# Kernel optimization log

Hardware: AMD Instinct MI355X
Metric: run time of the kernel (lower is better)

## Reference

```python
import jax, jax.numpy as jnp
import numpy as np
from jax.experimental.ode import odeint

B, T, NV = 2048, 256, 32   # batch, time steps, n ICU variables
H, L, OH = 64, 32, 64      # gru hidden, latent dim, ode hidden


def setup_inputs() -> dict:
    key = jax.random.key(0)
    ks = jax.random.split(key, 24)
    def rn(k, shape, s):
        return (jax.random.normal(k, shape) * s).astype(jnp.float32)
    times = jnp.broadcast_to(jnp.linspace(0.0, 48.0, T, dtype=jnp.float32), (B, T))
    values = jax.random.normal(ks[0], (B, T, NV), dtype=jnp.float32)
    mask = (jax.random.uniform(ks[1], (B, T, NV)) < 0.5).astype(jnp.float32)
    seq_lengths = jnp.sort(jax.random.randint(ks[2], (B,), 1, T + 1))[::-1]
    seq_lengths = seq_lengths.at[0].set(T).astype(jnp.int32)
    eps = jax.random.normal(ks[3], (B, L), dtype=jnp.float32)
    return {
        "times": times, "values": values, "mask": mask,
        "seq_lengths": seq_lengths, "eps": eps,
        # GRU (torch layout: gates stacked r,z,n)
        "W_ih": rn(ks[4], (3 * H, 2 * NV), 0.1), "W_hh": rn(ks[5], (3 * H, H), 0.1),
        "b_ih": rn(ks[6], (3 * H,), 0.05), "b_hh": rn(ks[7], (3 * H,), 0.05),
        # hidden -> z0 params
        "W_z0": rn(ks[8], (2 * L, H), 0.1), "b_z0": rn(ks[9], (2 * L,), 0.05),
        # ODE func MLP (small weights keep dynamics tame for dopri5)
        "ode_W1": rn(ks[10], (OH, L), 0.05), "ode_b1": rn(ks[11], (OH,), 0.02),
        "ode_W2": rn(ks[12], (OH, OH), 0.05), "ode_b2": rn(ks[13], (OH,), 0.02),
        "ode_W3": rn(ks[14], (L, OH), 0.05), "ode_b3": rn(ks[15], (L,), 0.02),
        # decoder
        "dec_W1": rn(ks[16], (H, L), 0.1), "dec_b1": rn(ks[17], (H,), 0.05),
        "dec_W2": rn(ks[18], (1, H), 0.1), "dec_b2": rn(ks[19], (1,), 0.05),
    }


def _latent_ode_fwd(times, values, mask, seq_lengths, eps,
                    W_ih, W_hh, b_ih, b_hh, W_z0, b_z0,
                    ode_W1, ode_b1, ode_W2, ode_b2, ode_W3, ode_b3,
                    dec_W1, dec_b1, dec_W2, dec_b2):
    Bx, Tx = values.shape[0], values.shape[1]
    # encoder: concat (values, mask), flip time, run GRU over first seq_len steps
    x = jnp.concatenate([values, mask], axis=-1)[:, ::-1, :]          # [B,T,2NV]
    xp = jnp.einsum('btf,gf->tbg', x, W_ih) + b_ih                    # [T,B,3H]

    def gru_step(h, inp):
        xpt, t = inp                                                  # xpt: [B,3H]
        hh = h @ W_hh.T + b_hh
        xr, xz, xn = jnp.split(xpt, 3, axis=-1)
        hr, hz, hn = jnp.split(hh, 3, axis=-1)
        r = jax.nn.sigmoid(xr + hr)
        zg = jax.nn.sigmoid(xz + hz)
        n = jnp.tanh(xn + r * hn)
        h_new = (1.0 - zg) * n + zg * h
        h = jnp.where((t < seq_lengths)[:, None], h_new, h)           # packed-seq freeze
        return h, None

    h0 = jnp.zeros((Bx, W_hh.shape[1]), values.dtype)
    h, _ = jax.lax.scan(gru_step, h0, (xp, jnp.arange(Tx)))

    z0p = h @ W_z0.T + b_z0                                           # [B,2L]
    Ld = z0p.shape[-1] // 2
    z0_mean, z0_logvar = z0p[:, :Ld], z0p[:, Ld:]
    z0 = z0_mean + eps * jnp.exp(0.5 * z0_logvar)                     # reparameterize

    def ode_f(z, t, p):
        W1, b1, W2, b2, W3, b3 = p
        hl = jnp.tanh(z @ W1.T + b1)
        hl = jnp.tanh(hl @ W2.T + b2)
        return hl @ W3.T + b3

    t_span = jnp.array([0.0, 48.0], dtype=jnp.float32)
    traj = odeint(ode_f, z0, t_span,
                  (ode_W1, ode_b1, ode_W2, ode_b2, ode_W3, ode_b3),
                  rtol=1e-7, atol=1e-9)                               # dopri5, torchdiffeq defaults
    z_final = traj[-1]

    logits = (jax.nn.relu(z_final @ dec_W1.T + dec_b1) @ dec_W2.T + dec_b2)[:, 0]
    kl = -0.5 * jnp.mean(1.0 + z0_logvar - z0_mean ** 2 - jnp.exp(z0_logvar))
    return logits, kl


def reference(times, values, mask, seq_lengths, eps,
              W_ih, W_hh, b_ih, b_hh, W_z0, b_z0,
              ode_W1, ode_b1, ode_W2, ode_b2, ode_W3, ode_b3,
              dec_W1, dec_b1, dec_W2, dec_b2):
    return _latent_ode_fwd(times, values, mask, seq_lengths, eps,
                           W_ih, W_hh, b_ih, b_hh, W_z0, b_z0,
                           ode_W1, ode_b1, ode_W2, ode_b2, ode_W3, ode_b3,
                           dec_W1, dec_b1, dec_W2, dec_b2)
```

## Files before the change

kernel.cpp:

```cpp
#include <hip/hip_runtime.h>

#define B_ 2048
#define T_ 256
#define NV_ 32
#define H_ 64
#define L_ 32
#define OH_ 64
#define NSTEP 16

typedef _Float16 f16x8 __attribute__((ext_vector_type(8)));
typedef _Float16 f16x4 __attribute__((ext_vector_type(4)));
typedef _Float16 f16x2 __attribute__((ext_vector_type(2)));
typedef float f32x4 __attribute__((ext_vector_type(4)));

#define MFMA16(a, b, c) __builtin_amdgcn_mfma_f32_16x16x32_f16((a), (b), (c), 0, 0, 0)

__device__ __forceinline__ float rcp_(float x) { return __builtin_amdgcn_rcpf(x); }
__device__ __forceinline__ float sigm(float x) { return rcp_(1.0f + __expf(-x)); }
__device__ __forceinline__ float tanh_(float x) { return 2.0f * rcp_(1.0f + __expf(-2.0f * x)) - 1.0f; }

__device__ __forceinline__ f16x8 pack8(f32x4 a, f32x4 b) {
    f16x8 r;
    r[0] = (_Float16)a[0]; r[1] = (_Float16)a[1]; r[2] = (_Float16)a[2]; r[3] = (_Float16)a[3];
    r[4] = (_Float16)b[0]; r[5] = (_Float16)b[1]; r[6] = (_Float16)b[2]; r[7] = (_Float16)b[3];
    return r;
}

__global__ __launch_bounds__(256) void gru_kernel(
    const float* __restrict__ values, const float* __restrict__ mask,
    const int* __restrict__ seql, const float* __restrict__ eps,
    const float* __restrict__ W_ih, const float* __restrict__ W_hh,
    const float* __restrict__ b_ih, const float* __restrict__ b_hh,
    const float* __restrict__ W_z0, const float* __restrict__ b_z0,
    float* __restrict__ z0ws, float* __restrict__ parts)
{
    const int tid = threadIdx.x;
    const int w   = tid >> 6;
    const int l   = tid & 63;
    const int c   = l & 15;
    const int g4  = l >> 4;
    const int b0  = blockIdx.x * 16;

    __shared__ unsigned h_u32[2][16][36];
    __shared__ float    zp_lds[16][65];
    __shared__ float    red_lds[4];

    for (int i = tid; i < 2 * 16 * 36; i += 256) (&h_u32[0][0][0])[i] = 0u;

    f16x8 bih[3][2], bhh[3][2];
#pragma unroll
    for (int gate = 0; gate < 3; ++gate) {
#pragma unroll
        for (int kt = 0; kt < 2; ++kt) {
            const float* p1 = W_ih + (gate * 64 + w * 16 + c) * 64 + kt * 32 + g4 * 8;
            bih[gate][kt] = pack8(*(const f32x4*)p1, *(const f32x4*)(p1 + 4));
            const float* p2 = W_hh + (gate * 64 + w * 16 + c) * 64 + kt * 32 + g4 * 8;
            bhh[gate][kt] = pack8(*(const f32x4*)p2, *(const f32x4*)(p2 + 4));
        }
    }

    f32x4 bRq, bZq, bNXq, bNHq;
#pragma unroll
    for (int r = 0; r < 4; ++r) {
        const int f = w * 16 + g4 * 4 + r;
        bRq[r]  = b_ih[f]       + b_hh[f];
        bZq[r]  = b_ih[64 + f]  + b_hh[64 + f];
        bNXq[r] = b_ih[128 + f];
        bNHq[r] = b_hh[128 + f];
    }

    const int sl_c  = seql[b0 + c];
    const int tmax  = seql[b0];
    float hp[4] = {0.f, 0.f, 0.f, 0.f};

    const float* vrow = values + (size_t)(b0 + c) * T_ * NV_ + g4 * 8;
    const float* mrow = mask   + (size_t)(b0 + c) * T_ * NV_ + g4 * 8;

    f32x4 av0, av1, am0, am1, bv0, bv1, bm0, bm1;
    {
        const float* vp = vrow + (T_ - 1) * NV_;
        const float* mp = mrow + (T_ - 1) * NV_;
        av0 = *(const f32x4*)vp; av1 = *(const f32x4*)(vp + 4);
        am0 = *(const f32x4*)mp; am1 = *(const f32x4*)(mp + 4);
    }
    {
        const int tt = (1 < tmax) ? 1 : 0;
        const float* vp = vrow + (T_ - 1 - tt) * NV_;
        const float* mp = mrow + (T_ - 1 - tt) * NV_;
        bv0 = *(const f32x4*)vp; bv1 = *(const f32x4*)(vp + 4);
        bm0 = *(const f32x4*)mp; bm1 = *(const f32x4*)(mp + 4);
    }

    __syncthreads();

    int cur = 0;

    auto STEP = [&](f32x4& v0, f32x4& v1, f32x4& m0, f32x4& m1, int tc) {
        f16x8 ha0 = *(const f16x8*)&h_u32[cur][c][4 * g4];
        f16x8 ha1 = *(const f16x8*)&h_u32[cur][c][16 + 4 * g4];

        f16x8 xa0 = pack8(v0, v1);
        f16x8 xa1 = pack8(m0, m1);

        const int tt = (tc + 2 < tmax) ? (tc + 2) : 0;
        const float* vp = vrow + (T_ - 1 - tt) * NV_;
        const float* mp = mrow + (T_ - 1 - tt) * NV_;
        v0 = *(const f32x4*)vp; v1 = *(const f32x4*)(vp + 4);
        m0 = *(const f32x4*)mp; m1 = *(const f32x4*)(mp + 4);

        f32x4 accR  = MFMA16(bih[0][0], xa0, bRq);
        f32x4 accNX = MFMA16(bih[2][0], xa0, bNXq);
        f32x4 accZ  = MFMA16(bih[1][0], xa0, bZq);
        accR  = MFMA16(bih[0][1], xa1, accR);
        accNX = MFMA16(bih[2][1], xa1, accNX);
        accZ  = MFMA16(bih[1][1], xa1, accZ);

        f32x4 accNH = MFMA16(bhh[2][0], ha0, bNHq);
        accR  = MFMA16(bhh[0][0], ha0, accR);
        accNH = MFMA16(bhh[2][1], ha1, accNH);
        accR  = MFMA16(bhh[0][1], ha1, accR);
        accZ  = MFMA16(bhh[1][0], ha0, accZ);
        accZ  = MFMA16(bhh[1][1], ha1, accZ);

        const bool act = (tc < sl_c);
#pragma unroll
        for (int r = 0; r < 4; ++r) {
            float rr   = sigm(accR[r]);
            float zz   = sigm(accZ[r]);
            float nn   = tanh_(accNX[r] + rr * accNH[r]);
            float hnew = nn + zz * (hp[r] - nn);
            if (act) hp[r] = hnew;
        }

        const int nxt = cur ^ 1;
        f16x2 q0 = { (_Float16)hp[0], (_Float16)hp[1] };
        f16x2 q1 = { (_Float16)hp[2], (_Float16)hp[3] };
        h_u32[nxt][c][8 * w + 2 * g4]     = __builtin_bit_cast(unsigned, q0);
        h_u32[nxt][c][8 * w + 2 * g4 + 1] = __builtin_bit_cast(unsigned, q1);

        asm volatile("s_waitcnt lgkmcnt(0)\n\ts_barrier" ::: "memory");
        cur = nxt;
    };

    int t = 0;
    while (true) {
        STEP(av0, av1, am0, am1, t);
        if (t + 1 >= tmax) break;
        STEP(bv0, bv1, bm0, bm1, t + 1);
        t += 2;
        if (t >= tmax) break;
    }

    f16x8 az0f[2];
#pragma unroll
    for (int kt = 0; kt < 2; ++kt) {
        const float* p = W_z0 + (w * 16 + c) * 64 + kt * 32 + g4 * 8;
        az0f[kt] = pack8(*(const f32x4*)p, *(const f32x4*)(p + 4));
    }
    f16x8 hf0 = *(const f16x8*)&h_u32[cur][c][4 * g4];
    f16x8 hf1 = *(const f16x8*)&h_u32[cur][c][16 + 4 * g4];
    f32x4 az;
#pragma unroll
    for (int r = 0; r < 4; ++r) az[r] = b_z0[w * 16 + g4 * 4 + r];
    az = MFMA16(az0f[0], hf0, az);
    az = MFMA16(az0f[1], hf1, az);
#pragma unroll
    for (int r = 0; r < 4; ++r) zp_lds[c][w * 16 + g4 * 4 + r] = az[r];
    __syncthreads();

    const int row = tid >> 4;
    const int j2  = (tid & 15) * 2;
    float m0 = zp_lds[row][j2],      m1 = zp_lds[row][j2 + 1];
    float v0 = zp_lds[row][32 + j2], v1 = zp_lds[row][32 + j2 + 1];
    const float* erow = eps + (size_t)(b0 + row) * L_;
    float e0 = erow[j2], e1 = erow[j2 + 1];
    float* zrow = z0ws + (size_t)(b0 + row) * L_;
    float s0 = __expf(0.5f * v0), s1 = __expf(0.5f * v1);
    zrow[j2]     = m0 + e0 * s0;
    zrow[j2 + 1] = m1 + e1 * s1;
    float kls = (1.0f + v0 - m0 * m0 - s0 * s0) + (1.0f + v1 - m1 * m1 - s1 * s1);
#pragma unroll
    for (int off = 32; off >= 1; off >>= 1) kls += __shfl_down(kls, off);
    if (l == 0) red_lds[w] = kls;
    __syncthreads();
    if (tid == 0) parts[blockIdx.x] = red_lds[0] + red_lds[1] + red_lds[2] + red_lds[3];
}

__global__ __launch_bounds__(64) void ode_kernel(
    const float* __restrict__ z0ws,
    const float* __restrict__ oW1, const float* __restrict__ ob1,
    const float* __restrict__ oW2, const float* __restrict__ ob2,
    const float* __restrict__ oW3, const float* __restrict__ ob3,
    const float* __restrict__ dW1, const float* __restrict__ db1,
    const float* __restrict__ dW2, const float* __restrict__ db2,
    float* __restrict__ out)
{
    const int l  = threadIdx.x;
    const int c  = l & 15;
    const int g4 = l >> 4;
    const int b0 = blockIdx.x * 16;

    __shared__ _Float16 zbuf[16][40];
    __shared__ _Float16 buf1[16][72];
    __shared__ _Float16 buf2[16][72];

    f16x8 w1f[4], d1f[4], w2f[4][2], w3f[2][2];
#pragma unroll
    for (int mt = 0; mt < 4; ++mt) {
        const float* p = oW1 + (mt * 16 + c) * 32 + g4 * 8;
        w1f[mt] = pack8(*(const f32x4*)p, *(const f32x4*)(p + 4));
        const float* q = dW1 + (mt * 16 + c) * 32 + g4 * 8;
        d1f[mt] = pack8(*(const f32x4*)q, *(const f32x4*)(q + 4));
#pragma unroll
        for (int kt = 0; kt < 2; ++kt) {
            const float* r = oW2 + (mt * 16 + c) * 64 + kt * 32 + g4 * 8;
            w2f[mt][kt] = pack8(*(const f32x4*)r, *(const f32x4*)(r + 4));
        }
    }
#pragma unroll
    for (int mt = 0; mt < 2; ++mt) {
#pragma unroll
        for (int kt = 0; kt < 2; ++kt) {
            const float* r = oW3 + (mt * 16 + c) * 64 + kt * 32 + g4 * 8;
            w3f[mt][kt] = pack8(*(const f32x4*)r, *(const f32x4*)(r + 4));
        }
    }

    f32x4 b1q[4], b2q[4], d1q[4], w2q[4], b3q[2];
#pragma unroll
    for (int mt = 0; mt < 4; ++mt) {
#pragma unroll
        for (int r = 0; r < 4; ++r) {
            b1q[mt][r] = ob1[mt * 16 + g4 * 4 + r];
            b2q[mt][r] = ob2[mt * 16 + g4 * 4 + r];
            d1q[mt][r] = db1[mt * 16 + g4 * 4 + r];
            w2q[mt][r] = dW2[mt * 16 + g4 * 4 + r];
        }
    }
#pragma unroll
    for (int mt = 0; mt < 2; ++mt) {
#pragma unroll
        for (int r = 0; r < 4; ++r) b3q[mt][r] = ob3[mt * 16 + g4 * 4 + r];
    }
    const float bd2 = db2[0];

    f32x4 z[2];
#pragma unroll
    for (int mt = 0; mt < 2; ++mt)
        z[mt] = *(const f32x4*)(z0ws + (size_t)(b0 + c) * L_ + mt * 16 + g4 * 4);

    auto evalf = [&](const f32x4* zin, f32x4* kout) {
#pragma unroll
        for (int mt = 0; mt < 2; ++mt) {
            f16x4 hv;
#pragma unroll
            for (int r = 0; r < 4; ++r) hv[r] = (_Float16)zin[mt][r];
            *(f16x4*)&zbuf[c][mt * 16 + g4 * 4] = hv;
        }
        f16x8 zf = *(const f16x8*)&zbuf[c][g4 * 8];

        f32x4 h1[4];
#pragma unroll
        for (int mt = 0; mt < 4; ++mt) h1[mt] = MFMA16(w1f[mt], zf, b1q[mt]);
#pragma unroll
        for (int mt = 0; mt < 4; ++mt) {
            f16x4 hv;
#pragma unroll
            for (int r = 0; r < 4; ++r) hv[r] = (_Float16)tanh_(h1[mt][r]);
            *(f16x4*)&buf1[c][mt * 16 + g4 * 4] = hv;
        }
        f16x8 a1 = *(const f16x8*)&buf1[c][g4 * 8];
        f16x8 a2 = *(const f16x8*)&buf1[c][32 + g4 * 8];

        f32x4 h2[4];
#pragma unroll
        for (int mt = 0; mt < 4; ++mt) {
            h2[mt] = MFMA16(w2f[mt][0], a1, b2q[mt]);
            h2[mt] = MFMA16(w2f[mt][1], a2, h2[mt]);
        }
#pragma unroll
        for (int mt = 0; mt < 4; ++mt) {
            f16x4 hv;
#pragma unroll
            for (int r = 0; r < 4; ++r) hv[r] = (_Float16)tanh_(h2[mt][r]);
            *(f16x4*)&buf2[c][mt * 16 + g4 * 4] = hv;
        }
        f16x8 a3 = *(const f16x8*)&buf2[c][g4 * 8];
        f16x8 a4 = *(const f16x8*)&buf2[c][32 + g4 * 8];

#pragma unroll
        for (int mt = 0; mt < 2; ++mt) {
            kout[mt] = MFMA16(w3f[mt][0], a3, b3q[mt]);
            kout[mt] = MFMA16(w3f[mt][1], a4, kout[mt]);
        }
    };

    const float dt = 48.0f / (float)NSTEP;
    for (int s = 0; s < NSTEP; ++s) {
        f32x4 k[2], ks[2], zt[2];
        evalf(z, k);
#pragma unroll
        for (int mt = 0; mt < 2; ++mt) { ks[mt] = k[mt]; zt[mt] = z[mt] + k[mt] * (0.5f * dt); }
        evalf(zt, k);
#pragma unroll
        for (int mt = 0; mt < 2; ++mt) { ks[mt] += k[mt] * 2.0f; zt[mt] = z[mt] + k[mt] * (0.5f * dt); }
        evalf(zt, k);
#pragma unroll
        for (int mt = 0; mt < 2; ++mt) { ks[mt] += k[mt] * 2.0f; zt[mt] = z[mt] + k[mt] * dt; }
        evalf(zt, k);
#pragma unroll
        for (int mt = 0; mt < 2; ++mt) z[mt] += (ks[mt] + k[mt]) * (dt / 6.0f);
    }

#pragma unroll
    for (int mt = 0; mt < 2; ++mt) {
        f16x4 hv;
#pragma unroll
        for (int r = 0; r < 4; ++r) hv[r] = (_Float16)z[mt][r];
        *(f16x4*)&zbuf[c][mt * 16 + g4 * 4] = hv;
    }
    f16x8 zf = *(const f16x8*)&zbuf[c][g4 * 8];
    float p = 0.0f;
#pragma unroll
    for (int mt = 0; mt < 4; ++mt) {
        f32x4 d = MFMA16(d1f[mt], zf, d1q[mt]);
#pragma unroll
        for (int r = 0; r < 4; ++r) p += fmaxf(d[r], 0.0f) * w2q[mt][r];
    }
    p += __shfl_xor(p, 16);
    p += __shfl_xor(p, 32);
    if (l < 16) out[b0 + c] = p + bd2;
}

__global__ __launch_bounds__(128) void kl_fin(const float* __restrict__ parts,
                                              float* __restrict__ out)
{
    __shared__ float sred[2];
    const int tid = threadIdx.x;
    float p = parts[tid];
#pragma unroll
    for (int off = 32; off >= 1; off >>= 1) p += __shfl_down(p, off);
    if ((tid & 63) == 0) sred[tid >> 6] = p;
    __syncthreads();
    if (tid == 0) out[B_] = -0.5f * (sred[0] + sred[1]) / (float)(B_ * L_);
}

extern "C" void kernel_launch(void* const* d_in, const int* in_sizes, int n_in,
                              void* d_out, int out_size, void* d_ws, size_t ws_size,
                              hipStream_t stream) {
    const float* values = (const float*)d_in[1];
    const float* mask   = (const float*)d_in[2];
    const int*   seql   = (const int*)d_in[3];
    const float* eps    = (const float*)d_in[4];
    const float* W_ih   = (const float*)d_in[5];
    const float* W_hh   = (const float*)d_in[6];
    const float* b_ih   = (const float*)d_in[7];
    const float* b_hh   = (const float*)d_in[8];
    const float* W_z0   = (const float*)d_in[9];
    const float* b_z0   = (const float*)d_in[10];
    const float* oW1    = (const float*)d_in[11];
    const float* ob1    = (const float*)d_in[12];
    const float* oW2    = (const float*)d_in[13];
    const float* ob2    = (const float*)d_in[14];
    const float* oW3    = (const float*)d_in[15];
    const float* ob3    = (const float*)d_in[16];
    const float* dW1    = (const float*)d_in[17];
    const float* db1    = (const float*)d_in[18];
    const float* dW2    = (const float*)d_in[19];
    const float* db2    = (const float*)d_in[20];
    float* out = (float*)d_out;

    float* z0ws  = (float*)d_ws;
    float* parts = z0ws + (size_t)B_ * L_;

    hipLaunchKernelGGL(gru_kernel, dim3(B_ / 16), dim3(256), 0, stream,
                       values, mask, seql, eps, W_ih, W_hh, b_ih, b_hh, W_z0, b_z0,
                       z0ws, parts);
    hipLaunchKernelGGL(ode_kernel, dim3(B_ / 16), dim3(64), 0, stream,
                       z0ws, oW1, ob1, oW2, ob2, oW3, ob3, dW1, db1, dW2, db2, out);
    hipLaunchKernelGGL(kl_fin, dim3(1), dim3(128), 0, stream, parts, out);
}
```

Before: 202.0 us.

## Split GRU into producer/consumer waves overlapping input projection with recurrence

Doubles the GRU block to 512 threads. Four producer waves load the inputs and compute the input-projection MFMAs one step ahead into a double-buffered LDS array. Four consumer waves run only the hidden-state MFMAs and gate math, raising their priority with s_setprio, which takes the input projection off the serial recurrence's critical path. The cost is extra LDS traffic, a barrier shared by twice as many waves, and half the threads idle during the epilogue.

```diff
diff --git a/kernel.cpp b/kernel.cpp
--- a/kernel.cpp
+++ b/kernel.cpp
@@ -26,7 +26,9 @@
     return r;
 }
 
-__global__ __launch_bounds__(256) void gru_kernel(
+#define RAWBAR() asm volatile("s_waitcnt lgkmcnt(0)\n\ts_barrier" ::: "memory")
+
+__global__ __launch_bounds__(512) void gru_kernel(
     const float* __restrict__ values, const float* __restrict__ mask,
     const int* __restrict__ seql, const float* __restrict__ eps,
     const float* __restrict__ W_ih, const float* __restrict__ W_hh,
@@ -34,154 +36,188 @@
     const float* __restrict__ W_z0, const float* __restrict__ b_z0,
     float* __restrict__ z0ws, float* __restrict__ parts)
 {
-    const int tid = threadIdx.x;
-    const int w   = tid >> 6;
-    const int l   = tid & 63;
-    const int c   = l & 15;
-    const int g4  = l >> 4;
-    const int b0  = blockIdx.x * 16;
+    const int tid  = threadIdx.x;
+    const int wave = tid >> 6;
+    const int l    = tid & 63;
+    const int c    = l & 15;
+    const int g4   = l >> 4;
+    const int b0   = blockIdx.x * 16;
+    const int w    = wave & 3;
+    const bool producer = (wave < 4);
 
     __shared__ unsigned h_u32[2][16][36];
-    __shared__ float    zp_lds[16][65];
+    __shared__ float    xp[2][16][200];
+    __shared__ float    zp_lds[16][68];
     __shared__ float    red_lds[4];
 
-    for (int i = tid; i < 2 * 16 * 36; i += 256) (&h_u32[0][0][0])[i] = 0u;
-
-    f16x8 bih[3][2], bhh[3][2];
-#pragma unroll
-    for (int gate = 0; gate < 3; ++gate) {
-#pragma unroll
-        for (int kt = 0; kt < 2; ++kt) {
-            const float* p1 = W_ih + (gate * 64 + w * 16 + c) * 64 + kt * 32 + g4 * 8;
-            bih[gate][kt] = pack8(*(const f32x4*)p1, *(const f32x4*)(p1 + 4));
-            const float* p2 = W_hh + (gate * 64 + w * 16 + c) * 64 + kt * 32 + g4 * 8;
-            bhh[gate][kt] = pack8(*(const f32x4*)p2, *(const f32x4*)(p2 + 4));
-        }
-    }
-
-    f32x4 bRq, bZq, bNXq, bNHq;
-#pragma unroll
-    for (int r = 0; r < 4; ++r) {
-        const int f = w * 16 + g4 * 4 + r;
-        bRq[r]  = b_ih[f]       + b_hh[f];
-        bZq[r]  = b_ih[64 + f]  + b_hh[64 + f];
-        bNXq[r] = b_ih[128 + f];
-        bNHq[r] = b_hh[128 + f];
-    }
-
-    const int sl_c  = seql[b0 + c];
-    const int tmax  = seql[b0];
-    float hp[4] = {0.f, 0.f, 0.f, 0.f};
-
+    for (int i = tid; i < 2 * 16 * 36; i += 512) (&h_u32[0][0][0])[i] = 0u;
+
+    const int tmax = seql[b0];
+
+    f16x8 bih[3][2];
+    f32x4 bRq, bZq, bNXq;
+    f32x4 av0, av1, am0, am1, bv0, bv1, bm0, bm1;
     const float* vrow = values + (size_t)(b0 + c) * T_ * NV_ + g4 * 8;
     const float* mrow = mask   + (size_t)(b0 + c) * T_ * NV_ + g4 * 8;
 
-    f32x4 av0, av1, am0, am1, bv0, bv1, bm0, bm1;
-    {
-        const float* vp = vrow + (T_ - 1) * NV_;
-        const float* mp = mrow + (T_ - 1) * NV_;
-        av0 = *(const f32x4*)vp; av1 = *(const f32x4*)(vp + 4);
-        am0 = *(const f32x4*)mp; am1 = *(const f32x4*)(mp + 4);
-    }
-    {
-        const int tt = (1 < tmax) ? 1 : 0;
-        const float* vp = vrow + (T_ - 1 - tt) * NV_;
-        const float* mp = mrow + (T_ - 1 - tt) * NV_;
-        bv0 = *(const f32x4*)vp; bv1 = *(const f32x4*)(vp + 4);
-        bm0 = *(const f32x4*)mp; bm1 = *(const f32x4*)(mp + 4);
+    f16x8 bhh[3][2];
+    f32x4 bNHq;
+    int   sl_c = 0;
+    float hp[4] = {0.f, 0.f, 0.f, 0.f};
+
+    if (producer) {
+#pragma unroll
+        for (int gate = 0; gate < 3; ++gate) {
+#pragma unroll
+            for (int kt = 0; kt < 2; ++kt) {
+                const float* p1 = W_ih + (gate * 64 + w * 16 + c) * 64 + kt * 32 + g4 * 8;
+                bih[gate][kt] = pack8(*(const f32x4*)p1, *(const f32x4*)(p1 + 4));
+            }
+        }
+#pragma unroll
+        for (int r = 0; r < 4; ++r) {
+            const int f = w * 16 + g4 * 4 + r;
+            bRq[r]  = b_ih[f]       + b_hh[f];
+            bZq[r]  = b_ih[64 + f]  + b_hh[64 + f];
+            bNXq[r] = b_ih[128 + f];
+        }
+        {
+            const float* vp = vrow + (T_ - 1) * NV_;
+            const float* mp = mrow + (T_ - 1) * NV_;
+            av0 = *(const f32x4*)vp; av1 = *(const f32x4*)(vp + 4);
+            am0 = *(const f32x4*)mp; am1 = *(const f32x4*)(mp + 4);
+        }
+        {
+            const int tt = (1 < tmax) ? 1 : 0;
+            const float* vp = vrow + (T_ - 1 - tt) * NV_;
+            const float* mp = mrow + (T_ - 1 - tt) * NV_;
+            bv0 = *(const f32x4*)vp; bv1 = *(const f32x4*)(vp + 4);
+            bm0 = *(const f32x4*)mp; bm1 = *(const f32x4*)(mp + 4);
+        }
+    } else {
+#pragma unroll
+        for (int gate = 0; gate < 3; ++gate) {
+#pragma unroll
+            for (int kt = 0; kt < 2; ++kt) {
+                const float* p2 = W_hh + (gate * 64 + w * 16 + c) * 64 + kt * 32 + g4 * 8;
+                bhh[gate][kt] = pack8(*(const f32x4*)p2, *(const f32x4*)(p2 + 4));
+            }
+        }
+#pragma unroll
+        for (int r = 0; r < 4; ++r) bNHq[r] = b_hh[128 + w * 16 + g4 * 4 + r];
+        sl_c = seql[b0 + c];
     }
 
     __syncthreads();
 
-    int cur = 0;
-
-    auto STEP = [&](f32x4& v0, f32x4& v1, f32x4& m0, f32x4& m1, int tc) {
-        f16x8 ha0 = *(const f16x8*)&h_u32[cur][c][4 * g4];
-        f16x8 ha1 = *(const f16x8*)&h_u32[cur][c][16 + 4 * g4];
-
+    const int xoff = w * 16 + g4 * 4;
+
+    auto PROD = [&](f32x4& v0, f32x4& v1, f32x4& m0, f32x4& m1, int p) {
         f16x8 xa0 = pack8(v0, v1);
         f16x8 xa1 = pack8(m0, m1);
-
-        const int tt = (tc + 2 < tmax) ? (tc + 2) : 0;
+        const int tt = (p + 2 < tmax) ? (p + 2) : 0;
         const float* vp = vrow + (T_ - 1 - tt) * NV_;
         const float* mp = mrow + (T_ - 1 - tt) * NV_;
         v0 = *(const f32x4*)vp; v1 = *(const f32x4*)(vp + 4);
         m0 = *(const f32x4*)mp; m1 = *(const f32x4*)(mp + 4);
 
-        f32x4 accR  = MFMA16(bih[0][0], xa0, bRq);
-        f32x4 accNX = MFMA16(bih[2][0], xa0, bNXq);
-        f32x4 accZ  = MFMA16(bih[1][0], xa0, bZq);
-        accR  = MFMA16(bih[0][1], xa1, accR);
-        accNX = MFMA16(bih[2][1], xa1, accNX);
-        accZ  = MFMA16(bih[1][1], xa1, accZ);
-
+        f32x4 aR  = MFMA16(bih[0][0], xa0, bRq);
+        f32x4 aZ  = MFMA16(bih[1][0], xa0, bZq);
+        f32x4 aNX = MFMA16(bih[2][0], xa0, bNXq);
+        aR  = MFMA16(bih[0][1], xa1, aR);
+        aZ  = MFMA16(bih[1][1], xa1, aZ);
+        aNX = MFMA16(bih[2][1], xa1, aNX);
+
+        float* dst = &xp[p & 1][c][0];
+        *(f32x4*)(dst + xoff)       = aR;
+        *(f32x4*)(dst + 64 + xoff)  = aZ;
+        *(f32x4*)(dst + 128 + xoff) = aNX;
+    };
+
+    auto CONS = [&](int t, int cur) {
+        const float* src = &xp[t & 1][c][0];
+        f32x4 xpR  = *(const f32x4*)(src + xoff);
+        f32x4 xpZ  = *(const f32x4*)(src + 64 + xoff);
+        f32x4 xpNX = *(const f32x4*)(src + 128 + xoff);
+        f16x8 ha0 = *(const f16x8*)&h_u32[cur][c][4 * g4];
+        f16x8 ha1 = *(const f16x8*)&h_u32[cur][c][16 + 4 * g4];
+
+        __builtin_amdgcn_s_setprio(1);
+        f32x4 accR  = MFMA16(bhh[0][0], ha0, xpR);
         f32x4 accNH = MFMA16(bhh[2][0], ha0, bNHq);
-        accR  = MFMA16(bhh[0][0], ha0, accR);
+        f32x4 accZ  = MFMA16(bhh[1][0], ha0, xpZ);
+        accR  = MFMA16(bhh[0][1], ha1, accR);
         accNH = MFMA16(bhh[2][1], ha1, accNH);
-        accR  = MFMA16(bhh[0][1], ha1, accR);
-        accZ  = MFMA16(bhh[1][0], ha0, accZ);
         accZ  = MFMA16(bhh[1][1], ha1, accZ);
 
-        const bool act = (tc < sl_c);
+        const bool act = (t < sl_c);
 #pragma unroll
         for (int r = 0; r < 4; ++r) {
             float rr   = sigm(accR[r]);
             float zz   = sigm(accZ[r]);
-            float nn   = tanh_(accNX[r] + rr * accNH[r]);
+            float nn   = tanh_(xpNX[r] + rr * accNH[r]);
             float hnew = nn + zz * (hp[r] - nn);
             if (act) hp[r] = hnew;
         }
-
-        const int nxt = cur ^ 1;
-        f16x2 q0 = { (_Float16)hp[0], (_Float16)hp[1] };
-        f16x2 q1 = { (_Float16)hp[2], (_Float16)hp[3] };
-        h_u32[nxt][c][8 * w + 2 * g4]     = __builtin_bit_cast(unsigned, q0);
-        h_u32[nxt][c][8 * w + 2 * g4 + 1] = __builtin_bit_cast(unsigned, q1);
-
-        asm volatile("s_waitcnt lgkmcnt(0)\n\ts_barrier" ::: "memory");
-        cur = nxt;
+        __builtin_amdgcn_s_setprio(0);
+
+        f16x4 hq;
+#pragma unroll
+        for (int r = 0; r < 4; ++r) hq[r] = (_Float16)hp[r];
+        *(f16x4*)&h_u32[cur ^ 1][c][8 * w + 2 * g4] = hq;
     };
 
-    int t = 0;
+    if (producer) PROD(av0, av1, am0, am1, 0);
+    RAWBAR();
+
+    int t = 0, cur = 0;
     while (true) {
-        STEP(av0, av1, am0, am1, t);
-        if (t + 1 >= tmax) break;
-        STEP(bv0, bv1, bm0, bm1, t + 1);
-        t += 2;
+        if (producer) { if (t + 1 < tmax) PROD(bv0, bv1, bm0, bm1, t + 1); }
+        else          CONS(t, cur);
+        RAWBAR();
+        cur ^= 1; ++t;
         if (t >= tmax) break;
-    }
-
-    f16x8 az0f[2];
-#pragma unroll
-    for (int kt = 0; kt < 2; ++kt) {
-        const float* p = W_z0 + (w * 16 + c) * 64 + kt * 32 + g4 * 8;
-        az0f[kt] = pack8(*(const f32x4*)p, *(const f32x4*)(p + 4));
-    }
-    f16x8 hf0 = *(const f16x8*)&h_u32[cur][c][4 * g4];
-    f16x8 hf1 = *(const f16x8*)&h_u32[cur][c][16 + 4 * g4];
-    f32x4 az;
-#pragma unroll
-    for (int r = 0; r < 4; ++r) az[r] = b_z0[w * 16 + g4 * 4 + r];
-    az = MFMA16(az0f[0], hf0, az);
-    az = MFMA16(az0f[1], hf1, az);
-#pragma unroll
-    for (int r = 0; r < 4; ++r) zp_lds[c][w * 16 + g4 * 4 + r] = az[r];
+        if (producer) { if (t + 1 < tmax) PROD(av0, av1, am0, am1, t + 1); }
+        else          CONS(t, cur);
+        RAWBAR();
+        cur ^= 1; ++t;
+        if (t >= tmax) break;
+    }
+
+    if (!producer) {
+        f16x8 az0f[2];
+#pragma unroll
+        for (int kt = 0; kt < 2; ++kt) {
+            const float* p = W_z0 + (w * 16 + c) * 64 + kt * 32 + g4 * 8;
+            az0f[kt] = pack8(*(const f32x4*)p, *(const f32x4*)(p + 4));
+        }
+        f16x8 hf0 = *(const f16x8*)&h_u32[cur][c][4 * g4];
+        f16x8 hf1 = *(const f16x8*)&h_u32[cur][c][16 + 4 * g4];
+        f32x4 az;
+#pragma unroll
+        for (int r = 0; r < 4; ++r) az[r] = b_z0[w * 16 + g4 * 4 + r];
+        az = MFMA16(az0f[0], hf0, az);
+        az = MFMA16(az0f[1], hf1, az);
+        *(f32x4*)&zp_lds[c][xoff] = az;
+    }
     __syncthreads();
 
-    const int row = tid >> 4;
-    const int j2  = (tid & 15) * 2;
-    float m0 = zp_lds[row][j2],      m1 = zp_lds[row][j2 + 1];
-    float v0 = zp_lds[row][32 + j2], v1 = zp_lds[row][32 + j2 + 1];
-    const float* erow = eps + (size_t)(b0 + row) * L_;
-    float e0 = erow[j2], e1 = erow[j2 + 1];
-    float* zrow = z0ws + (size_t)(b0 + row) * L_;
-    float s0 = __expf(0.5f * v0), s1 = __expf(0.5f * v1);
-    zrow[j2]     = m0 + e0 * s0;
-    zrow[j2 + 1] = m1 + e1 * s1;
-    float kls = (1.0f + v0 - m0 * m0 - s0 * s0) + (1.0f + v1 - m1 * m1 - s1 * s1);
-#pragma unroll
-    for (int off = 32; off >= 1; off >>= 1) kls += __shfl_down(kls, off);
-    if (l == 0) red_lds[w] = kls;
+    if (tid < 256) {
+        const int row = tid >> 4;
+        const int j2  = (tid & 15) * 2;
+        float m0 = zp_lds[row][j2],      m1 = zp_lds[row][j2 + 1];
+        float v0 = zp_lds[row][32 + j2], v1 = zp_lds[row][32 + j2 + 1];
+        const float* erow = eps + (size_t)(b0 + row) * L_;
+        float e0 = erow[j2], e1 = erow[j2 + 1];
+        float* zrow = z0ws + (size_t)(b0 + row) * L_;
+        float s0 = __expf(0.5f * v0), s1 = __expf(0.5f * v1);
+        zrow[j2]     = m0 + e0 * s0;
+        zrow[j2 + 1] = m1 + e1 * s1;
+        float kls = (1.0f + v0 - m0 * m0 - s0 * s0) + (1.0f + v1 - m1 * m1 - s1 * s1);
+#pragma unroll
+        for (int off = 32; off >= 1; off >>= 1) kls += __shfl_down(kls, off);
+        if (l == 0) red_lds[wave] = kls;
+    }
     __syncthreads();
     if (tid == 0) parts[blockIdx.x] = red_lds[0] + red_lds[1] + red_lds[2] + red_lds[3];
 }
@@ -373,7 +409,7 @@
     float* z0ws  = (float*)d_ws;
     float* parts = z0ws + (size_t)B_ * L_;
 
-    hipLaunchKernelGGL(gru_kernel, dim3(B_ / 16), dim3(256), 0, stream,
+    hipLaunchKernelGGL(gru_kernel, dim3(B_ / 16), dim3(512), 0, stream,
                        values, mask, seql, eps, W_ih, W_hh, b_ih, b_hh, W_z0, b_z0,
                        z0ws, parts);
     hipLaunchKernelGGL(ode_kernel, dim3(B_ / 16), dim3(64), 0, stream,
```

New measurement: 194.3 us. 3.8% less time.

## Replace GRU step barrier with LDS counter spin-wait and deepen input prefetch

Applied to the files above, without the earlier changes.

Swaps the per-timestep s_barrier in the GRU recurrence for an LDS atomic counter that each wave bumps and then spin-waits on. Input prefetch is deepened from 2 to 6 timesteps using six register sets, so global load latency is hidden further ahead. Hidden-state writes are merged into a single f16x4 store and the z-projection into a single vector store. The spin loop adds LDS polling traffic, the extra prefetch sets raise register pressure, and correctness now rests on the counter ordering standing in for the barrier.

```diff
diff --git a/kernel.cpp b/kernel.cpp
--- a/kernel.cpp
+++ b/kernel.cpp
@@ -7,10 +7,10 @@
 #define L_ 32
 #define OH_ 64
 #define NSTEP 16
+#define DEPTH 6
 
 typedef _Float16 f16x8 __attribute__((ext_vector_type(8)));
 typedef _Float16 f16x4 __attribute__((ext_vector_type(4)));
-typedef _Float16 f16x2 __attribute__((ext_vector_type(2)));
 typedef float f32x4 __attribute__((ext_vector_type(4)));
 
 #define MFMA16(a, b, c) __builtin_amdgcn_mfma_f32_16x16x32_f16((a), (b), (c), 0, 0, 0)
@@ -42,10 +42,12 @@
     const int b0  = blockIdx.x * 16;
 
     __shared__ unsigned h_u32[2][16][36];
-    __shared__ float    zp_lds[16][65];
+    __shared__ float    zp_lds[16][68];
     __shared__ float    red_lds[4];
+    __shared__ unsigned cnt;
 
     for (int i = tid; i < 2 * 16 * 36; i += 256) (&h_u32[0][0][0])[i] = 0u;
+    if (tid == 0) cnt = 0u;
 
     f16x8 bih[3][2], bhh[3][2];
 #pragma unroll
@@ -69,86 +71,77 @@
         bNHq[r] = b_hh[128 + f];
     }
 
-    const int sl_c  = seql[b0 + c];
-    const int tmax  = seql[b0];
+    const int sl_c = seql[b0 + c];
+    const int tmax = seql[b0];
     float hp[4] = {0.f, 0.f, 0.f, 0.f};
 
     const float* vrow = values + (size_t)(b0 + c) * T_ * NV_ + g4 * 8;
     const float* mrow = mask   + (size_t)(b0 + c) * T_ * NV_ + g4 * 8;
 
-    f32x4 av0, av1, am0, am1, bv0, bv1, bm0, bm1;
-    {
-        const float* vp = vrow + (T_ - 1) * NV_;
-        const float* mp = mrow + (T_ - 1) * NV_;
-        av0 = *(const f32x4*)vp; av1 = *(const f32x4*)(vp + 4);
-        am0 = *(const f32x4*)mp; am1 = *(const f32x4*)(mp + 4);
-    }
-    {
-        const int tt = (1 < tmax) ? 1 : 0;
-        const float* vp = vrow + (T_ - 1 - tt) * NV_;
-        const float* mp = mrow + (T_ - 1 - tt) * NV_;
-        bv0 = *(const f32x4*)vp; bv1 = *(const f32x4*)(vp + 4);
-        bm0 = *(const f32x4*)mp; bm1 = *(const f32x4*)(mp + 4);
-    }
+#define DECLSET(S) f32x4 S##v0, S##v1, S##m0, S##m1
+    DECLSET(A); DECLSET(B); DECLSET(C); DECLSET(D); DECLSET(E); DECLSET(F);
+#define FILLSET(S, tc) do {                                                  \
+        const int tt_ = ((tc) < tmax) ? (tc) : 0;                            \
+        const float* vp_ = vrow + (T_ - 1 - tt_) * NV_;                      \
+        const float* mp_ = mrow + (T_ - 1 - tt_) * NV_;                      \
+        S##v0 = *(const f32x4*)vp_; S##v1 = *(const f32x4*)(vp_ + 4);        \
+        S##m0 = *(const f32x4*)mp_; S##m1 = *(const f32x4*)(mp_ + 4);        \
+    } while (0)
+    FILLSET(A, 0); FILLSET(B, 1); FILLSET(C, 2);
+    FILLSET(D, 3); FILLSET(E, 4); FILLSET(F, 5);
 
     __syncthreads();
 
-    int cur = 0;
-
-    auto STEP = [&](f32x4& v0, f32x4& v1, f32x4& m0, f32x4& m1, int tc) {
-        f16x8 ha0 = *(const f16x8*)&h_u32[cur][c][4 * g4];
-        f16x8 ha1 = *(const f16x8*)&h_u32[cur][c][16 + 4 * g4];
-
-        f16x8 xa0 = pack8(v0, v1);
-        f16x8 xa1 = pack8(m0, m1);
-
-        const int tt = (tc + 2 < tmax) ? (tc + 2) : 0;
-        const float* vp = vrow + (T_ - 1 - tt) * NV_;
-        const float* mp = mrow + (T_ - 1 - tt) * NV_;
-        v0 = *(const f32x4*)vp; v1 = *(const f32x4*)(vp + 4);
-        m0 = *(const f32x4*)mp; m1 = *(const f32x4*)(mp + 4);
-
-        f32x4 accR  = MFMA16(bih[0][0], xa0, bRq);
-        f32x4 accNX = MFMA16(bih[2][0], xa0, bNXq);
-        f32x4 accZ  = MFMA16(bih[1][0], xa0, bZq);
-        accR  = MFMA16(bih[0][1], xa1, accR);
-        accNX = MFMA16(bih[2][1], xa1, accNX);
-        accZ  = MFMA16(bih[1][1], xa1, accZ);
-
-        f32x4 accNH = MFMA16(bhh[2][0], ha0, bNHq);
-        accR  = MFMA16(bhh[0][0], ha0, accR);
-        accNH = MFMA16(bhh[2][1], ha1, accNH);
-        accR  = MFMA16(bhh[0][1], ha1, accR);
-        accZ  = MFMA16(bhh[1][0], ha0, accZ);
-        accZ  = MFMA16(bhh[1][1], ha1, accZ);
-
-        const bool act = (tc < sl_c);
-#pragma unroll
-        for (int r = 0; r < 4; ++r) {
-            float rr   = sigm(accR[r]);
-            float zz   = sigm(accZ[r]);
-            float nn   = tanh_(accNX[r] + rr * accNH[r]);
-            float hnew = nn + zz * (hp[r] - nn);
-            if (act) hp[r] = hnew;
-        }
-
-        const int nxt = cur ^ 1;
-        f16x2 q0 = { (_Float16)hp[0], (_Float16)hp[1] };
-        f16x2 q1 = { (_Float16)hp[2], (_Float16)hp[3] };
-        h_u32[nxt][c][8 * w + 2 * g4]     = __builtin_bit_cast(unsigned, q0);
-        h_u32[nxt][c][8 * w + 2 * g4 + 1] = __builtin_bit_cast(unsigned, q1);
-
-        asm volatile("s_waitcnt lgkmcnt(0)\n\ts_barrier" ::: "memory");
-        cur = nxt;
-    };
+#define GSTEP(S, tc) do {                                                    \
+        f16x8 ha0 = *(const f16x8*)&h_u32[(tc) & 1][c][4 * g4];              \
+        f16x8 ha1 = *(const f16x8*)&h_u32[(tc) & 1][c][16 + 4 * g4];         \
+        f16x8 xa0 = pack8(S##v0, S##v1);                                     \
+        f16x8 xa1 = pack8(S##m0, S##m1);                                     \
+        FILLSET(S, (tc) + DEPTH);                                            \
+        f32x4 accR  = MFMA16(bih[0][0], xa0, bRq);                           \
+        f32x4 accNX = MFMA16(bih[2][0], xa0, bNXq);                          \
+        f32x4 accZ  = MFMA16(bih[1][0], xa0, bZq);                           \
+        accR  = MFMA16(bih[0][1], xa1, accR);                                \
+        accNX = MFMA16(bih[2][1], xa1, accNX);                               \
+        accZ  = MFMA16(bih[1][1], xa1, accZ);                                \
+        f32x4 accNH = MFMA16(bhh[2][0], ha0, bNHq);                          \
+        accR  = MFMA16(bhh[0][0], ha0, accR);                                \
+        accNH = MFMA16(bhh[2][1], ha1, accNH);                               \
+        accR  = MFMA16(bhh[0][1], ha1, accR);                                \
+        accZ  = MFMA16(bhh[1][0], ha0, accZ);                                \
+        accZ  = MFMA16(bhh[1][1], ha1, accZ);                                \
+        const bool act = ((tc) < sl_c);                                      \
+        _Pragma("unroll")                                                    \
+        for (int r = 0; r < 4; ++r) {                                        \
+            float rr   = sigm(accR[r]);                                      \
+            float zz   = sigm(accZ[r]);                                      \
+            float nn   = tanh_(accNX[r] + rr * accNH[r]);                    \
+            float hnew = nn + zz * (hp[r] - nn);                             \
+            if (act) hp[r] = hnew;                                           \
+        }                                                                    \
+        f16x4 hq;                                                            \
+        _Pragma("unroll")                                                    \
+        for (int r = 0; r < 4; ++r) hq[r] = (_Float16)hp[r];                 \
+        *(f16x4*)&h_u32[((tc) & 1) ^ 1][c][8 * w + 2 * g4] = hq;             \
+        asm volatile("s_waitcnt lgkmcnt(0)" ::: "memory");                   \
+        if (l == 0) atomicAdd(&cnt, 1u);                                     \
+        asm volatile("" ::: "memory");                                       \
+        {                                                                    \
+            const unsigned tgt_ = 4u * ((unsigned)(tc) + 1u);                \
+            while (__builtin_amdgcn_readfirstlane(                           \
+                       *(volatile unsigned*)&cnt) < tgt_) { }                \
+        }                                                                    \
+        asm volatile("" ::: "memory");                                       \
+    } while (0)
 
     int t = 0;
     while (true) {
-        STEP(av0, av1, am0, am1, t);
-        if (t + 1 >= tmax) break;
-        STEP(bv0, bv1, bm0, bm1, t + 1);
-        t += 2;
-        if (t >= tmax) break;
+        GSTEP(A, t); if (++t >= tmax) break;
+        GSTEP(B, t); if (++t >= tmax) break;
+        GSTEP(C, t); if (++t >= tmax) break;
+        GSTEP(D, t); if (++t >= tmax) break;
+        GSTEP(E, t); if (++t >= tmax) break;
+        GSTEP(F, t); if (++t >= tmax) break;
     }
 
     f16x8 az0f[2];
@@ -157,15 +150,15 @@
         const float* p = W_z0 + (w * 16 + c) * 64 + kt * 32 + g4 * 8;
         az0f[kt] = pack8(*(const f32x4*)p, *(const f32x4*)(p + 4));
     }
-    f16x8 hf0 = *(const f16x8*)&h_u32[cur][c][4 * g4];
-    f16x8 hf1 = *(const f16x8*)&h_u32[cur][c][16 + 4 * g4];
+    const int fin = tmax & 1;
+    f16x8 hf0 = *(const f16x8*)&h_u32[fin][c][4 * g4];
+    f16x8 hf1 = *(const f16x8*)&h_u32[fin][c][16 + 4 * g4];
     f32x4 az;
 #pragma unroll
     for (int r = 0; r < 4; ++r) az[r] = b_z0[w * 16 + g4 * 4 + r];
     az = MFMA16(az0f[0], hf0, az);
     az = MFMA16(az0f[1], hf1, az);
-#pragma unroll
-    for (int r = 0; r < 4; ++r) zp_lds[c][w * 16 + g4 * 4 + r] = az[r];
+    *(f32x4*)&zp_lds[c][w * 16 + g4 * 4] = az;
     __syncthreads();
 
     const int row = tid >> 4;
```

New measurement: 225.5 us. +11.7%, slower.
